# Performance work log

Measured on AMD Instinct MI355X. Metric: run time of the kernel, lower is better.

## Reference

```python
import jax, jax.numpy as jnp
import numpy as np

D = 1024
H = 16
DH = D // H  # 64


def setup_inputs() -> dict:
    key = jax.random.key(0)
    ks = jax.random.split(key, 7)
    X = jax.random.normal(ks[0], (2, 2048, D), dtype=jnp.float32)
    # Per-head projection weights stacked along head axis: [H, D, DH]
    s = 1.0 / np.sqrt(D)
    Wq = jax.random.uniform(ks[1], (H, D, DH), jnp.float32, -s, s)
    Wk = jax.random.uniform(ks[2], (H, D, DH), jnp.float32, -s, s)
    Wv = jax.random.uniform(ks[3], (H, D, DH), jnp.float32, -s, s)
    bq = jax.random.uniform(ks[4], (H, DH), jnp.float32, -s, s)
    bk = jax.random.uniform(ks[5], (H, DH), jnp.float32, -s, s)
    bv = jax.random.uniform(ks[6], (H, DH), jnp.float32, -s, s)
    return {"X": X, "Wq": Wq, "bq": bq, "Wk": Wk, "bk": bk, "Wv": Wv, "bv": bv}


def reference(X, Wq, bq, Wk, bk, Wv, bv):
    B, S, _ = X.shape
    # Per-head linear projections (batched over heads): [B, H, S, DH]
    Q = jnp.einsum('bsd,hde->bhse', X, Wq) + bq[None, :, None, :]
    K = jnp.einsum('bsd,hde->bhse', X, Wk) + bk[None, :, None, :]
    V = jnp.einsum('bsd,hde->bhse', X, Wv) + bv[None, :, None, :]
    scale = jnp.sqrt(jnp.asarray(DH, dtype=X.dtype))
    QK = jnp.einsum('bhse,bhte->bhst', Q, K) / scale  # [B, H, S, S]
    # Faithful to source: softmax over full row FIRST, then lower-tri mask
    # (post-softmax tril, no renormalization).
    sQK = jax.nn.softmax(QK, axis=-1)
    tril = jnp.tril(jnp.ones((S, S), dtype=X.dtype))
    sQK = sQK * tril
    out = jnp.einsum('bhst,bhte->bhse', sQK, V)  # [B, H, S, DH]
    # Concatenate heads along feature dim (torch.cat over per-head outputs)
    return out.transpose(0, 2, 1, 3).reshape(B, S, H * DH)
```

## Files before the change

### kernel.cpp

```cpp
#include <hip/hip_runtime.h>
#include <math.h>

#define B_  2
#define S_  2048
#define D_  1024
#define H_  16
#define DH_ 64

typedef unsigned short u16;
typedef unsigned int   u32;
typedef _Float16       f16;
typedef _Float16 half8  __attribute__((ext_vector_type(8)));
typedef _Float16 half4  __attribute__((ext_vector_type(4)));
typedef float    f32x4  __attribute__((ext_vector_type(4)));

#if __has_builtin(__builtin_amdgcn_exp2f)
#define EXP2(x) __builtin_amdgcn_exp2f(x)
#else
#define EXP2(x) exp2f(x)
#endif

__device__ __forceinline__ u16 h_bits(f16 h){ return __builtin_bit_cast(u16, h); }

__global__ __launch_bounds__(256) void prep_kernel(
    const float* __restrict__ X,
    const float* __restrict__ Wq, const float* __restrict__ Wk,
    const float* __restrict__ Wv,
    u16* __restrict__ Xhi, u16* __restrict__ Xlo, u16* __restrict__ Wt)
{
    __shared__ float Wf[64][65];
    const int bid = blockIdx.x;
    const int c   = threadIdx.x;

    if (bid < 4096){
        const int idx = bid * 256 + c;
        float4 v = ((const float4*)X)[idx];
        float fv[4] = {v.x, v.y, v.z, v.w};
        u16 hh[4], ll[4];
        #pragma unroll
        for (int j = 0; j < 4; ++j){
            f16 hi = (f16)fv[j];
            hh[j] = h_bits(hi);
            ll[j] = h_bits((f16)(fv[j] - (float)hi));
        }
        uint2 ph, pl;
        ph.x = hh[0] | ((u32)hh[1] << 16);
        ph.y = hh[2] | ((u32)hh[3] << 16);
        pl.x = ll[0] | ((u32)ll[1] << 16);
        pl.y = ll[2] | ((u32)ll[3] << 16);
        ((uint2*)Xhi)[idx] = ph;
        ((uint2*)Xlo)[idx] = pl;
        return;
    }

    const int wb = bid - 4096;
    const int d0 = (wb & 15) * 64;
    const int h  = (wb >> 4) & 15;
    const int which = wb >> 8;
    const float* src = (which == 0) ? Wq : (which == 1) ? Wk : Wv;
    src += (size_t)h * D_ * DH_;

    #pragma unroll
    for (int it = 0; it < 4; ++it){
        int d  = (c >> 4) + 16 * it;
        int e4 = (c & 15) * 4;
        float4 v = *(const float4*)(src + (size_t)(d0 + d) * DH_ + e4);
        Wf[d][e4+0] = v.x; Wf[d][e4+1] = v.y; Wf[d][e4+2] = v.z; Wf[d][e4+3] = v.w;
    }
    __syncthreads();
    u16* dst = Wt + (size_t)(which * H_ + h) * DH_ * D_;
    #pragma unroll
    for (int it = 0; it < 4; ++it){
        int e  = (c >> 4) + 16 * it;
        int d4 = (c & 15) * 4;
        u16 q[4];
        #pragma unroll
        for (int j = 0; j < 4; ++j)
            q[j] = h_bits((f16)(Wf[d4 + j][e] * 64.0f));
        u32* p = (u32*)(dst + (size_t)e * D_ + d0 + d4);
        p[0] = q[0] | ((u32)q[1] << 16);
        p[1] = q[2] | ((u32)q[3] << 16);
    }
}

#define PKS 40

__global__ __launch_bounds__(256, 3) void proj_kernel(
    const u16* __restrict__ Xhi, const u16* __restrict__ Xlo,
    const u16* __restrict__ Wt,
    const float* __restrict__ bq, const float* __restrict__ bk,
    const float* __restrict__ bv,
    f16* __restrict__ Qh, f16* __restrict__ Kh, f16* __restrict__ Vt)
{
    __shared__ u16 XsHi[128 * PKS], XsLo[128 * PKS], Bs[128 * PKS];

    const int tid  = threadIdx.x;
    const int lane = tid & 63;
    const int w    = tid >> 6;
    const int quad = lane >> 4;
    const int ln   = lane & 15;
    const int wr   = (w >> 1) * 64;
    const int wc   = (w & 1) * 64;
    const int m0   = blockIdx.x * 128;
    const int c0   = blockIdx.y * 128;

    const int sr  = tid >> 2;
    const int sch = (tid & 3) * 8;

    const u16* xh0 = Xhi + (size_t)(m0 + sr) * D_ + sch;
    const u16* xh1 = xh0 + (size_t)64 * D_;
    const u16* xl0 = Xlo + (size_t)(m0 + sr) * D_ + sch;
    const u16* xl1 = xl0 + (size_t)64 * D_;
    const u16* wb0 = Wt  + (size_t)(c0 + sr) * D_ + sch;
    const u16* wb1 = wb0 + (size_t)64 * D_;

    uint4 rh0 = *(const uint4*)xh0, rh1 = *(const uint4*)xh1;
    uint4 rl0 = *(const uint4*)xl0, rl1 = *(const uint4*)xl1;
    uint4 rw0 = *(const uint4*)wb0, rw1 = *(const uint4*)wb1;

    f32x4 acc[4][4];
    #pragma unroll
    for (int i = 0; i < 4; ++i)
        #pragma unroll
        for (int j = 0; j < 4; ++j)
            acc[i][j] = (f32x4){0.f, 0.f, 0.f, 0.f};

    for (int k0 = 0; k0 < D_; k0 += 32){
        __syncthreads();
        *(uint4*)&XsHi[sr * PKS + sch]        = rh0;
        *(uint4*)&XsHi[(sr + 64) * PKS + sch] = rh1;
        *(uint4*)&XsLo[sr * PKS + sch]        = rl0;
        *(uint4*)&XsLo[(sr + 64) * PKS + sch] = rl1;
        *(uint4*)&Bs[sr * PKS + sch]          = rw0;
        *(uint4*)&Bs[(sr + 64) * PKS + sch]   = rw1;
        const int kn = k0 + 32;
        if (kn < D_){
            rh0 = *(const uint4*)(xh0 + kn); rh1 = *(const uint4*)(xh1 + kn);
            rl0 = *(const uint4*)(xl0 + kn); rl1 = *(const uint4*)(xl1 + kn);
            rw0 = *(const uint4*)(wb0 + kn); rw1 = *(const uint4*)(wb1 + kn);
        }
        __syncthreads();

        half8 ahi[4], alo[4], bf[4];
        #pragma unroll
        for (int mt = 0; mt < 4; ++mt){
            int row = wr + 16 * mt + ln;
            ahi[mt] = __builtin_bit_cast(half8, *(const uint4*)&XsHi[row * PKS + quad * 8]);
            alo[mt] = __builtin_bit_cast(half8, *(const uint4*)&XsLo[row * PKS + quad * 8]);
        }
        #pragma unroll
        for (int nt = 0; nt < 4; ++nt)
            bf[nt] = __builtin_bit_cast(half8,
                *(const uint4*)&Bs[(wc + 16 * nt + ln) * PKS + quad * 8]);
        #pragma unroll
        for (int mt = 0; mt < 4; ++mt)
            #pragma unroll
            for (int nt = 0; nt < 4; ++nt){
                acc[mt][nt] = __builtin_amdgcn_mfma_f32_16x16x32_f16(ahi[mt], bf[nt], acc[mt][nt], 0, 0, 0);
                acc[mt][nt] = __builtin_amdgcn_mfma_f32_16x16x32_f16(alo[mt], bf[nt], acc[mt][nt], 0, 0, 0);
            }
    }

    const float QSCALE = 0.125f * 1.44269504088896340736f;
    const float INV64  = 0.015625f;
    #pragma unroll
    for (int nt = 0; nt < 4; ++nt){
        int colg  = c0 + wc + 16 * nt + ln;
        int which = colg >> 10;
        int h     = (colg >> 6) & 15;
        int e     = colg & 63;
        const float* bp = (which == 0) ? bq : (which == 1) ? bk : bv;
        float bias = bp[h * DH_ + e];
        if (which < 2){
            f16* op = (which == 0) ? Qh : Kh;
            float scale = (which == 0) ? QSCALE : 1.0f;
            #pragma unroll
            for (int mt = 0; mt < 4; ++mt)
                #pragma unroll
                for (int r = 0; r < 4; ++r){
                    int sg = m0 + wr + 16 * mt + 4 * quad + r;
                    int b  = sg >> 11;
                    int s  = sg & (S_ - 1);
                    float val = (acc[mt][nt][r] * INV64 + bias) * scale;
                    op[((size_t)(b * H_ + h) * S_ + s) * DH_ + e] = (f16)val;
                }
        } else {
            #pragma unroll
            for (int mt = 0; mt < 4; ++mt){
                int sg0 = m0 + wr + 16 * mt + 4 * quad;
                int b   = sg0 >> 11;
                int s0  = sg0 & (S_ - 1);
                u16 p[4];
                #pragma unroll
                for (int r = 0; r < 4; ++r)
                    p[r] = h_bits((f16)(acc[mt][nt][r] * INV64 + bias));
                uint2 pk;
                pk.x = p[0] | ((u32)p[1] << 16);
                pk.y = p[2] | ((u32)p[3] << 16);
                *(uint2*)((u16*)Vt + ((size_t)((b * H_ + h) * DH_ + e)) * S_ + s0) = pk;
            }
        }
    }
}

#define AKS 72

__global__ __launch_bounds__(256, 4) void attn_kernel(
    const f16* __restrict__ Qh, const f16* __restrict__ Kh,
    const f16* __restrict__ Vt, float* __restrict__ Out)
{
    __shared__ u16 Ks[64 * AKS];
    __shared__ u16 Vs[64 * AKS];

    const int tid  = threadIdx.x;
    const int lane = tid & 63;
    const int w    = tid >> 6;
    const int quad = lane >> 4;
    const int ln   = lane & 15;
    const int hb   = blockIdx.x;
    const int i    = blockIdx.y;
    const int h    = hb & 15;
    const int b    = hb >> 4;
    const int bh   = hb;
    const int sub  = w & 1;
    const int qbase = (w >> 1) ? (S_ - 32 * (i + 1) + 16 * sub)
                               : (32 * i + 16 * sub);
    const int vmax  = S_ - 32 * i - 1;

    const u16* Qg = (const u16*)Qh + (size_t)bh * S_ * DH_;
    const u16* Kg = (const u16*)Kh + (size_t)bh * S_ * DH_;
    const u16* Vg = (const u16*)Vt + (size_t)bh * DH_ * S_;

    half8 qf[2];
    #pragma unroll
    for (int ks = 0; ks < 2; ++ks)
        qf[ks] = __builtin_bit_cast(half8,
            *(const uint4*)(Qg + (size_t)(qbase + ln) * DH_ + 32 * ks + 8 * quad));

    const int kr = tid >> 3;
    const int kc = (tid & 7) * 8;

    uint4 kA = *(const uint4*)(Kg + (size_t)kr * DH_ + kc);
    uint4 kB = *(const uint4*)(Kg + (size_t)(kr + 32) * DH_ + kc);
    uint4 vA = *(const uint4*)(Vg + (size_t)kr * S_ + kc);
    uint4 vB = *(const uint4*)(Vg + (size_t)(kr + 32) * S_ + kc);

    float l_r = 0.f;
    f32x4 o_acc[4];
    #pragma unroll
    for (int nt = 0; nt < 4; ++nt) o_acc[nt] = (f32x4){0.f, 0.f, 0.f, 0.f};

    const int qrow   = qbase + ln;
    const int pv_lim = qbase + 15;

    for (int t0 = 0; t0 < S_; t0 += 64){
        __syncthreads();
        *(uint4*)&Ks[kr * AKS + kc]        = kA;
        *(uint4*)&Ks[(kr + 32) * AKS + kc] = kB;
        if (t0 <= vmax){
            *(uint4*)&Vs[kr * AKS + kc]        = vA;
            *(uint4*)&Vs[(kr + 32) * AKS + kc] = vB;
        }
        const int tn = t0 + 64;
        if (tn < S_){
            kA = *(const uint4*)(Kg + (size_t)(tn + kr) * DH_ + kc);
            kB = *(const uint4*)(Kg + (size_t)(tn + kr + 32) * DH_ + kc);
            if (tn <= vmax){
                vA = *(const uint4*)(Vg + (size_t)kr * S_ + tn + kc);
                vB = *(const uint4*)(Vg + (size_t)(kr + 32) * S_ + tn + kc);
            }
        }
        __syncthreads();

        f32x4 sc[4];
        #pragma unroll
        for (int mt = 0; mt < 4; ++mt) sc[mt] = (f32x4){0.f, 0.f, 0.f, 0.f};
        #pragma unroll
        for (int ks = 0; ks < 2; ++ks)
            #pragma unroll
            for (int mt = 0; mt < 4; ++mt){
                half8 kf = __builtin_bit_cast(half8,
                    *(const uint4*)&Ks[(16 * mt + ln) * AKS + 32 * ks + 8 * quad]);
                sc[mt] = __builtin_amdgcn_mfma_f32_16x16x32_f16(kf, qf[ks], sc[mt], 0, 0, 0);
            }

        #pragma unroll
        for (int mt = 0; mt < 4; ++mt)
            #pragma unroll
            for (int r = 0; r < 4; ++r)
                sc[mt][r] = EXP2(sc[mt][r]);
        float s = ((sc[0][0] + sc[0][1] + sc[0][2] + sc[0][3]) +
                   (sc[1][0] + sc[1][1] + sc[1][2] + sc[1][3])) +
                  ((sc[2][0] + sc[2][1] + sc[2][2] + sc[2][3]) +
                   (sc[3][0] + sc[3][1] + sc[3][2] + sc[3][3]));
        s += __shfl_xor(s, 16);
        s += __shfl_xor(s, 32);
        l_r += s;

        #pragma unroll
        for (int mt = 0; mt < 4; ++mt){
            const int ts = t0 + 16 * mt;
            if (ts <= pv_lim){
                half4 pf;
                if (ts == qbase){
                    int tb = ts + 4 * quad;
                    #pragma unroll
                    for (int r = 0; r < 4; ++r)
                        pf[r] = (tb + r > qrow) ? (f16)0.f : (f16)sc[mt][r];
                } else {
                    #pragma unroll
                    for (int r = 0; r < 4; ++r)
                        pf[r] = (f16)sc[mt][r];
                }
                #pragma unroll
                for (int nt = 0; nt < 4; ++nt){
                    half4 vf = __builtin_bit_cast(half4,
                        *(const uint2*)&Vs[(16 * nt + ln) * AKS + 16 * mt + 4 * quad]);
                    o_acc[nt] = __builtin_amdgcn_mfma_f32_16x16x16f16(pf, vf, o_acc[nt], 0, 0, 0);
                }
            }
        }
    }

    #pragma unroll
    for (int r = 0; r < 4; ++r){
        float lv  = __shfl(l_r, (lane & 48) | (4 * quad + r));
        float inv = 1.0f / lv;
        int sg = qbase + 4 * quad + r;
        float* op = Out + ((size_t)b * S_ + sg) * D_ + h * DH_;
        #pragma unroll
        for (int nt = 0; nt < 4; ++nt)
            op[16 * nt + ln] = o_acc[nt][r] * inv;
    }
}

extern "C" void kernel_launch(void* const* d_in, const int* in_sizes, int n_in,
                              void* d_out, int out_size, void* d_ws, size_t ws_size,
                              hipStream_t stream)
{
    const float* X  = (const float*)d_in[0];
    const float* Wq = (const float*)d_in[1];
    const float* bq = (const float*)d_in[2];
    const float* Wk = (const float*)d_in[3];
    const float* bk = (const float*)d_in[4];
    const float* Wv = (const float*)d_in[5];
    const float* bv = (const float*)d_in[6];
    float* out = (float*)d_out;

    u16* Wt  = (u16*)d_ws;
    f16* Qh  = (f16*)(Wt + 3145728);
    f16* Kh  = Qh + 4194304;
    f16* Vt  = Kh + 4194304;
    u16* Xhi = (u16*)(Vt + 4194304);
    u16* Xlo = Xhi + 4194304;

    prep_kernel<<<dim3(4096 + 768), 256, 0, stream>>>(X, Wq, Wk, Wv, Xhi, Xlo, Wt);
    proj_kernel<<<dim3(32, 24), 256, 0, stream>>>(Xhi, Xlo, Wt, bq, bk, bv, Qh, Kh, Vt);
    attn_kernel<<<dim3(32, 32), 256, 0, stream>>>(Qh, Kh, Vt, out);
}
```

Baseline: 189.2 us.

## Restructure projection GEMM with 256x256 tiles and direct-to-LDS double-buffered loads

The projection kernel now uses 512-thread blocks that each compute a 256x256 output tile, and a 1D grid with a block-index swizzle. Tiles are staged straight into XOR-swizzled LDS with global_load_lds, double-buffered across K steps, with explicit vmcnt waits, raw barriers and raised wave priority around MFMA bursts. The hi and lo halves of X are handled as one concatenated K loop. The goal is more data reuse per loaded byte and fewer LDS bank conflicts. In exchange, 128KB of LDS per block and only 192 blocks may leave many CUs idle.

```diff
diff --git a/kernel.cpp b/kernel.cpp
--- a/kernel.cpp
+++ b/kernel.cpp
@@ -83,89 +83,153 @@
     }
 }
 
-#define PKS 40
-
-__global__ __launch_bounds__(256, 3) void proj_kernel(
+__device__ __forceinline__ void gload16(const void* g, void* l){
+    __builtin_amdgcn_global_load_lds(
+        (const __attribute__((address_space(1))) void*)g,
+        (__attribute__((address_space(3))) void*)l, 16, 0, 0);
+}
+
+__device__ __forceinline__ half8 frag16(const char* hb, int row, int quad){
+    int off = row * 64 + ((quad * 16) ^ ((row & 6) << 3));
+    return __builtin_bit_cast(half8, *(const uint4*)(hb + off));
+}
+
+#define FENCE() asm volatile("" ::: "memory")
+#define BARX()  do{ FENCE(); __builtin_amdgcn_s_barrier(); FENCE(); }while(0)
+#define WAIT_VM4() asm volatile("s_waitcnt vmcnt(4)" ::: "memory")
+#define WAIT_VM0() asm volatile("s_waitcnt vmcnt(0)" ::: "memory")
+
+#define STAGE_A(t_, kh_) do{ \
+    const int _t = (t_); \
+    const int _gk = ((_t & 15) << 6) + ((kh_) << 5); \
+    const u16* _g0 = ((_t < 16) ? xa0h : xa0l) + _gk; \
+    const u16* _g1 = ((_t < 16) ? xa1h : xa1l) + _gk; \
+    char* _l = AsB + ((_t & 1) << 15) + ((kh_) << 14); \
+    gload16(_g0, _l + ldw0); \
+    gload16(_g1, _l + ldw1); \
+}while(0)
+
+#define STAGE_B(t_, kh_) do{ \
+    const int _t = (t_); \
+    const int _gk = ((_t & 15) << 6) + ((kh_) << 5); \
+    char* _l = BsB + ((_t & 1) << 15) + ((kh_) << 14); \
+    gload16(wb0 + _gk, _l + ldw0); \
+    gload16(wb1 + _gk, _l + ldw1); \
+}while(0)
+
+#define READ_B(bh_) do{ \
+    _Pragma("unroll") \
+    for (int nf_ = 0; nf_ < 4; ++nf_) \
+        bfr[nf_] = frag16((bh_), wn * 64 + nf_ * 16 + ln, quad); \
+}while(0)
+
+#define READ_A(ah_, mbase_) do{ \
+    _Pragma("unroll") \
+    for (int mi_ = 0; mi_ < 4; ++mi_) \
+        af[mi_] = frag16((ah_), wm * 128 + ((mbase_) + mi_) * 16 + ln, quad); \
+}while(0)
+
+#define MFMA_BLOCK(mbase_) do{ \
+    BARX(); \
+    asm volatile("s_waitcnt lgkmcnt(0)" ::: "memory"); \
+    __builtin_amdgcn_sched_barrier(0); \
+    __builtin_amdgcn_s_setprio(1); \
+    _Pragma("unroll") \
+    for (int mi_ = 0; mi_ < 4; ++mi_){ \
+        _Pragma("unroll") \
+        for (int nf_ = 0; nf_ < 4; ++nf_) \
+            acc[(mbase_) + mi_][nf_] = __builtin_amdgcn_mfma_f32_16x16x32_f16( \
+                af[mi_], bfr[nf_], acc[(mbase_) + mi_][nf_], 0, 0, 0); \
+    } \
+    __builtin_amdgcn_s_setprio(0); \
+}while(0)
+
+__global__ __launch_bounds__(512, 2) void proj_kernel(
     const u16* __restrict__ Xhi, const u16* __restrict__ Xlo,
     const u16* __restrict__ Wt,
     const float* __restrict__ bq, const float* __restrict__ bk,
     const float* __restrict__ bv,
     f16* __restrict__ Qh, f16* __restrict__ Kh, f16* __restrict__ Vt)
 {
-    __shared__ u16 XsHi[128 * PKS], XsLo[128 * PKS], Bs[128 * PKS];
+    __shared__ __align__(16) char AsB[65536];
+    __shared__ __align__(16) char BsB[65536];
 
     const int tid  = threadIdx.x;
     const int lane = tid & 63;
     const int w    = tid >> 6;
+    const int wm   = w >> 2;
+    const int wn   = w & 3;
     const int quad = lane >> 4;
     const int ln   = lane & 15;
-    const int wr   = (w >> 1) * 64;
-    const int wc   = (w & 1) * 64;
-    const int m0   = blockIdx.x * 128;
-    const int c0   = blockIdx.y * 128;
-
-    const int sr  = tid >> 2;
-    const int sch = (tid & 3) * 8;
-
-    const u16* xh0 = Xhi + (size_t)(m0 + sr) * D_ + sch;
-    const u16* xh1 = xh0 + (size_t)64 * D_;
-    const u16* xl0 = Xlo + (size_t)(m0 + sr) * D_ + sch;
-    const u16* xl1 = xl0 + (size_t)64 * D_;
-    const u16* wb0 = Wt  + (size_t)(c0 + sr) * D_ + sch;
-    const u16* wb1 = wb0 + (size_t)64 * D_;
-
-    uint4 rh0 = *(const uint4*)xh0, rh1 = *(const uint4*)xh1;
-    uint4 rl0 = *(const uint4*)xl0, rl1 = *(const uint4*)xl1;
-    uint4 rw0 = *(const uint4*)wb0, rw1 = *(const uint4*)wb1;
-
-    f32x4 acc[4][4];
-    #pragma unroll
-    for (int i = 0; i < 4; ++i)
+
+    const int bid = blockIdx.x;
+    const int swz = (bid & 7) * 24 + (bid >> 3);
+    const int m0  = (swz / 12) * 256;
+    const int c0  = (swz % 12) * 256;
+
+    const int Lr0 = w * 1024 + lane * 16;
+    const int Lr1 = (8 + w) * 1024 + lane * 16;
+    const int P0  = Lr0 ^ (((Lr0 >> 7) & 3) << 4);
+    const int P1  = Lr1 ^ (((Lr1 >> 7) & 3) << 4);
+    const int row0 = P0 >> 6,        row1 = P1 >> 6;
+    const int ko0  = (P0 & 63) >> 1, ko1  = (P1 & 63) >> 1;
+
+    const u16* xa0h = Xhi + (size_t)(m0 + row0) * D_ + ko0;
+    const u16* xa1h = Xhi + (size_t)(m0 + row1) * D_ + ko1;
+    const u16* xa0l = Xlo + (size_t)(m0 + row0) * D_ + ko0;
+    const u16* xa1l = Xlo + (size_t)(m0 + row1) * D_ + ko1;
+    const u16* wb0  = Wt  + (size_t)(c0 + row0) * D_ + ko0;
+    const u16* wb1  = Wt  + (size_t)(c0 + row1) * D_ + ko1;
+
+    const int ldw0 = w * 1024;
+    const int ldw1 = (8 + w) * 1024;
+
+    f32x4 acc[8][4];
+    #pragma unroll
+    for (int i = 0; i < 8; ++i)
         #pragma unroll
         for (int j = 0; j < 4; ++j)
             acc[i][j] = (f32x4){0.f, 0.f, 0.f, 0.f};
 
-    for (int k0 = 0; k0 < D_; k0 += 32){
-        __syncthreads();
-        *(uint4*)&XsHi[sr * PKS + sch]        = rh0;
-        *(uint4*)&XsHi[(sr + 64) * PKS + sch] = rh1;
-        *(uint4*)&XsLo[sr * PKS + sch]        = rl0;
-        *(uint4*)&XsLo[(sr + 64) * PKS + sch] = rl1;
-        *(uint4*)&Bs[sr * PKS + sch]          = rw0;
-        *(uint4*)&Bs[(sr + 64) * PKS + sch]   = rw1;
-        const int kn = k0 + 32;
-        if (kn < D_){
-            rh0 = *(const uint4*)(xh0 + kn); rh1 = *(const uint4*)(xh1 + kn);
-            rl0 = *(const uint4*)(xl0 + kn); rl1 = *(const uint4*)(xl1 + kn);
-            rw0 = *(const uint4*)(wb0 + kn); rw1 = *(const uint4*)(wb1 + kn);
-        }
-        __syncthreads();
-
-        half8 ahi[4], alo[4], bf[4];
-        #pragma unroll
-        for (int mt = 0; mt < 4; ++mt){
-            int row = wr + 16 * mt + ln;
-            ahi[mt] = __builtin_bit_cast(half8, *(const uint4*)&XsHi[row * PKS + quad * 8]);
-            alo[mt] = __builtin_bit_cast(half8, *(const uint4*)&XsLo[row * PKS + quad * 8]);
-        }
-        #pragma unroll
-        for (int nt = 0; nt < 4; ++nt)
-            bf[nt] = __builtin_bit_cast(half8,
-                *(const uint4*)&Bs[(wc + 16 * nt + ln) * PKS + quad * 8]);
-        #pragma unroll
-        for (int mt = 0; mt < 4; ++mt)
-            #pragma unroll
-            for (int nt = 0; nt < 4; ++nt){
-                acc[mt][nt] = __builtin_amdgcn_mfma_f32_16x16x32_f16(ahi[mt], bf[nt], acc[mt][nt], 0, 0, 0);
-                acc[mt][nt] = __builtin_amdgcn_mfma_f32_16x16x32_f16(alo[mt], bf[nt], acc[mt][nt], 0, 0, 0);
-            }
+    STAGE_A(0, 0); STAGE_B(0, 0); STAGE_A(0, 1); STAGE_B(0, 1);
+    STAGE_A(1, 0); STAGE_B(1, 0);
+    WAIT_VM4();
+    BARX();
+
+    half8 bfr[4], af[4];
+
+    #pragma unroll 2
+    for (int t = 0; t < 32; ++t){
+        const char* Ah = AsB + ((t & 1) << 15);
+        const char* Bh = BsB + ((t & 1) << 15);
+
+        READ_B(Bh); READ_A(Ah, 0);
+        if (t < 31) STAGE_A(t + 1, 1);
+        MFMA_BLOCK(0);
+        BARX();
+
+        READ_A(Ah, 4);
+        if (t < 31) STAGE_B(t + 1, 1);
+        MFMA_BLOCK(4);
+        BARX();
+
+        READ_B(Bh + 16384); READ_A(Ah + 16384, 0);
+        if (t < 30) STAGE_A(t + 2, 0);
+        MFMA_BLOCK(0);
+        BARX();
+
+        READ_A(Ah + 16384, 4);
+        if (t < 30) STAGE_B(t + 2, 0);
+        MFMA_BLOCK(4);
+        if (t < 30) { WAIT_VM4(); } else { WAIT_VM0(); }
+        BARX();
     }
 
     const float QSCALE = 0.125f * 1.44269504088896340736f;
     const float INV64  = 0.015625f;
     #pragma unroll
-    for (int nt = 0; nt < 4; ++nt){
-        int colg  = c0 + wc + 16 * nt + ln;
+    for (int nf = 0; nf < 4; ++nf){
+        int colg  = c0 + wn * 64 + nf * 16 + ln;
         int which = colg >> 10;
         int h     = (colg >> 6) & 15;
         int e     = colg & 63;
@@ -175,25 +239,25 @@
             f16* op = (which == 0) ? Qh : Kh;
             float scale = (which == 0) ? QSCALE : 1.0f;
             #pragma unroll
-            for (int mt = 0; mt < 4; ++mt)
+            for (int mf = 0; mf < 8; ++mf)
                 #pragma unroll
                 for (int r = 0; r < 4; ++r){
-                    int sg = m0 + wr + 16 * mt + 4 * quad + r;
+                    int sg = m0 + wm * 128 + mf * 16 + 4 * quad + r;
                     int b  = sg >> 11;
                     int s  = sg & (S_ - 1);
-                    float val = (acc[mt][nt][r] * INV64 + bias) * scale;
+                    float val = (acc[mf][nf][r] * INV64 + bias) * scale;
                     op[((size_t)(b * H_ + h) * S_ + s) * DH_ + e] = (f16)val;
                 }
         } else {
             #pragma unroll
-            for (int mt = 0; mt < 4; ++mt){
-                int sg0 = m0 + wr + 16 * mt + 4 * quad;
+            for (int mf = 0; mf < 8; ++mf){
+                int sg0 = m0 + wm * 128 + mf * 16 + 4 * quad;
                 int b   = sg0 >> 11;
                 int s0  = sg0 & (S_ - 1);
                 u16 p[4];
                 #pragma unroll
                 for (int r = 0; r < 4; ++r)
-                    p[r] = h_bits((f16)(acc[mt][nt][r] * INV64 + bias));
+                    p[r] = h_bits((f16)(acc[mf][nf][r] * INV64 + bias));
                 uint2 pk;
                 pk.x = p[0] | ((u32)p[1] << 16);
                 pk.y = p[2] | ((u32)p[3] << 16);
@@ -355,6 +419,6 @@
     u16* Xlo = Xhi + 4194304;
 
     prep_kernel<<<dim3(4096 + 768), 256, 0, stream>>>(X, Wq, Wk, Wv, Xhi, Xlo, Wt);
-    proj_kernel<<<dim3(32, 24), 256, 0, stream>>>(Xhi, Xlo, Wt, bq, bk, bv, Qh, Kh, Vt);
+    proj_kernel<<<dim3(192), dim3(512), 0, stream>>>(Xhi, Xlo, Wt, bq, bk, bv, Qh, Kh, Vt);
     attn_kernel<<<dim3(32, 32), 256, 0, stream>>>(Qh, Kh, Vt, out);
 }
```

New measurement: 199.4 us. 1.05x slower.

## Process 32 query rows per wave in attention to reuse K/V tiles

Applied to the files above, without the earlier changes.

Each wave in the attention kernel now handles two 16-row query groups instead of one. Each K fragment read from shared memory feeds two QK MFMAs, and each V fragment feeds two PV MFMAs. The grid is halved and launch bounds drop to 2 blocks per CU to make room for the doubled accumulators. This lowers the number of K/V global loads and LDS reads per unit of work, at the cost of fewer resident waves and fewer blocks (512) to spread across CUs.

```diff
diff --git a/kernel.cpp b/kernel.cpp
--- a/kernel.cpp
+++ b/kernel.cpp
@@ -205,7 +205,7 @@
 
 #define AKS 72
 
-__global__ __launch_bounds__(256, 4) void attn_kernel(
+__global__ __launch_bounds__(256, 2) void attn_kernel(
     const f16* __restrict__ Qh, const f16* __restrict__ Kh,
     const f16* __restrict__ Vt, float* __restrict__ Out)
 {
@@ -223,19 +223,22 @@
     const int b    = hb >> 4;
     const int bh   = hb;
     const int sub  = w & 1;
-    const int qbase = (w >> 1) ? (S_ - 32 * (i + 1) + 16 * sub)
-                               : (32 * i + 16 * sub);
-    const int vmax  = S_ - 32 * i - 1;
+    const int qbase = (w >> 1) ? (S_ - 64 * (i + 1) + 32 * sub)
+                               : (64 * i + 32 * sub);
+    const int vmax  = S_ - 64 * i - 1;
 
     const u16* Qg = (const u16*)Qh + (size_t)bh * S_ * DH_;
     const u16* Kg = (const u16*)Kh + (size_t)bh * S_ * DH_;
     const u16* Vg = (const u16*)Vt + (size_t)bh * DH_ * S_;
 
-    half8 qf[2];
-    #pragma unroll
-    for (int ks = 0; ks < 2; ++ks)
-        qf[ks] = __builtin_bit_cast(half8,
+    half8 qf0[2], qf1[2];
+    #pragma unroll
+    for (int ks = 0; ks < 2; ++ks){
+        qf0[ks] = __builtin_bit_cast(half8,
             *(const uint4*)(Qg + (size_t)(qbase + ln) * DH_ + 32 * ks + 8 * quad));
+        qf1[ks] = __builtin_bit_cast(half8,
+            *(const uint4*)(Qg + (size_t)(qbase + 16 + ln) * DH_ + 32 * ks + 8 * quad));
+    }
 
     const int kr = tid >> 3;
     const int kc = (tid & 7) * 8;
@@ -245,13 +248,18 @@
     uint4 vA = *(const uint4*)(Vg + (size_t)kr * S_ + kc);
     uint4 vB = *(const uint4*)(Vg + (size_t)(kr + 32) * S_ + kc);
 
-    float l_r = 0.f;
-    f32x4 o_acc[4];
-    #pragma unroll
-    for (int nt = 0; nt < 4; ++nt) o_acc[nt] = (f32x4){0.f, 0.f, 0.f, 0.f};
-
-    const int qrow   = qbase + ln;
-    const int pv_lim = qbase + 15;
+    float l0 = 0.f, l1 = 0.f;
+    f32x4 oa0[4], oa1[4];
+    #pragma unroll
+    for (int nt = 0; nt < 4; ++nt){
+        oa0[nt] = (f32x4){0.f, 0.f, 0.f, 0.f};
+        oa1[nt] = (f32x4){0.f, 0.f, 0.f, 0.f};
+    }
+
+    const int qrow0 = qbase + ln;
+    const int qrow1 = qbase + 16 + ln;
+    const int pvl0  = qbase + 15;
+    const int pvl1  = qbase + 31;
 
     for (int t0 = 0; t0 < S_; t0 += 64){
         __syncthreads();
@@ -272,51 +280,82 @@
         }
         __syncthreads();
 
-        f32x4 sc[4];
-        #pragma unroll
-        for (int mt = 0; mt < 4; ++mt) sc[mt] = (f32x4){0.f, 0.f, 0.f, 0.f};
+        f32x4 s0[4], s1[4];
+        #pragma unroll
+        for (int mt = 0; mt < 4; ++mt){
+            s0[mt] = (f32x4){0.f, 0.f, 0.f, 0.f};
+            s1[mt] = (f32x4){0.f, 0.f, 0.f, 0.f};
+        }
         #pragma unroll
         for (int ks = 0; ks < 2; ++ks)
             #pragma unroll
             for (int mt = 0; mt < 4; ++mt){
                 half8 kf = __builtin_bit_cast(half8,
                     *(const uint4*)&Ks[(16 * mt + ln) * AKS + 32 * ks + 8 * quad]);
-                sc[mt] = __builtin_amdgcn_mfma_f32_16x16x32_f16(kf, qf[ks], sc[mt], 0, 0, 0);
+                s0[mt] = __builtin_amdgcn_mfma_f32_16x16x32_f16(kf, qf0[ks], s0[mt], 0, 0, 0);
+                s1[mt] = __builtin_amdgcn_mfma_f32_16x16x32_f16(kf, qf1[ks], s1[mt], 0, 0, 0);
             }
 
         #pragma unroll
         for (int mt = 0; mt < 4; ++mt)
             #pragma unroll
-            for (int r = 0; r < 4; ++r)
-                sc[mt][r] = EXP2(sc[mt][r]);
-        float s = ((sc[0][0] + sc[0][1] + sc[0][2] + sc[0][3]) +
-                   (sc[1][0] + sc[1][1] + sc[1][2] + sc[1][3])) +
-                  ((sc[2][0] + sc[2][1] + sc[2][2] + sc[2][3]) +
-                   (sc[3][0] + sc[3][1] + sc[3][2] + sc[3][3]));
-        s += __shfl_xor(s, 16);
-        s += __shfl_xor(s, 32);
-        l_r += s;
+            for (int r = 0; r < 4; ++r){
+                s0[mt][r] = EXP2(s0[mt][r]);
+                s1[mt][r] = EXP2(s1[mt][r]);
+            }
+        {
+            float sa = ((s0[0][0] + s0[0][1] + s0[0][2] + s0[0][3]) +
+                        (s0[1][0] + s0[1][1] + s0[1][2] + s0[1][3])) +
+                       ((s0[2][0] + s0[2][1] + s0[2][2] + s0[2][3]) +
+                        (s0[3][0] + s0[3][1] + s0[3][2] + s0[3][3]));
+            sa += __shfl_xor(sa, 16);
+            sa += __shfl_xor(sa, 32);
+            l0 += sa;
+            float sb = ((s1[0][0] + s1[0][1] + s1[0][2] + s1[0][3]) +
+                        (s1[1][0] + s1[1][1] + s1[1][2] + s1[1][3])) +
+                       ((s1[2][0] + s1[2][1] + s1[2][2] + s1[2][3]) +
+                        (s1[3][0] + s1[3][1] + s1[3][2] + s1[3][3]));
+            sb += __shfl_xor(sb, 16);
+            sb += __shfl_xor(sb, 32);
+            l1 += sb;
+        }
 
         #pragma unroll
         for (int mt = 0; mt < 4; ++mt){
             const int ts = t0 + 16 * mt;
-            if (ts <= pv_lim){
-                half4 pf;
-                if (ts == qbase){
+            if (ts <= pvl1){
+                const int g0on = (ts <= pvl0);
+                half4 pf1;
+                if (ts == qbase + 16){
                     int tb = ts + 4 * quad;
                     #pragma unroll
                     for (int r = 0; r < 4; ++r)
-                        pf[r] = (tb + r > qrow) ? (f16)0.f : (f16)sc[mt][r];
+                        pf1[r] = (tb + r > qrow1) ? (f16)0.f : (f16)s1[mt][r];
                 } else {
                     #pragma unroll
                     for (int r = 0; r < 4; ++r)
-                        pf[r] = (f16)sc[mt][r];
+                        pf1[r] = (f16)s1[mt][r];
+                }
+                half4 pf0;
+                if (g0on){
+                    if (ts == qbase){
+                        int tb = ts + 4 * quad;
+                        #pragma unroll
+                        for (int r = 0; r < 4; ++r)
+                            pf0[r] = (tb + r > qrow0) ? (f16)0.f : (f16)s0[mt][r];
+                    } else {
+                        #pragma unroll
+                        for (int r = 0; r < 4; ++r)
+                            pf0[r] = (f16)s0[mt][r];
+                    }
                 }
                 #pragma unroll
                 for (int nt = 0; nt < 4; ++nt){
                     half4 vf = __builtin_bit_cast(half4,
                         *(const uint2*)&Vs[(16 * nt + ln) * AKS + 16 * mt + 4 * quad]);
-                    o_acc[nt] = __builtin_amdgcn_mfma_f32_16x16x16f16(pf, vf, o_acc[nt], 0, 0, 0);
+                    oa1[nt] = __builtin_amdgcn_mfma_f32_16x16x16f16(pf1, vf, oa1[nt], 0, 0, 0);
+                    if (g0on)
+                        oa0[nt] = __builtin_amdgcn_mfma_f32_16x16x16f16(pf0, vf, oa0[nt], 0, 0, 0);
                 }
             }
         }
@@ -324,13 +363,21 @@
 
     #pragma unroll
     for (int r = 0; r < 4; ++r){
-        float lv  = __shfl(l_r, (lane & 48) | (4 * quad + r));
-        float inv = 1.0f / lv;
-        int sg = qbase + 4 * quad + r;
-        float* op = Out + ((size_t)b * S_ + sg) * D_ + h * DH_;
+        float lv0  = __shfl(l0, (lane & 48) | (4 * quad + r));
+        float inv0 = 1.0f / lv0;
+        int sg0 = qbase + 4 * quad + r;
+        float* op0 = Out + ((size_t)b * S_ + sg0) * D_ + h * DH_;
         #pragma unroll
         for (int nt = 0; nt < 4; ++nt)
-            op[16 * nt + ln] = o_acc[nt][r] * inv;
+            op0[16 * nt + ln] = oa0[nt][r] * inv0;
+
+        float lv1  = __shfl(l1, (lane & 48) | (4 * quad + r));
+        float inv1 = 1.0f / lv1;
+        int sg1 = qbase + 16 + 4 * quad + r;
+        float* op1 = Out + ((size_t)b * S_ + sg1) * D_ + h * DH_;
+        #pragma unroll
+        for (int nt = 0; nt < 4; ++nt)
+            op1[16 * nt + ln] = oa1[nt][r] * inv1;
     }
 }
 
@@ -356,5 +403,5 @@
 
     prep_kernel<<<dim3(4096 + 768), 256, 0, stream>>>(X, Wq, Wk, Wv, Xhi, Xlo, Wt);
     proj_kernel<<<dim3(32, 24), 256, 0, stream>>>(Xhi, Xlo, Wt, bq, bk, bv, Qh, Kh, Vt);
-    attn_kernel<<<dim3(32, 32), 256, 0, stream>>>(Qh, Kh, Vt, out);
+    attn_kernel<<<dim3(32, 16), 256, 0, stream>>>(Qh, Kh, Vt, out);
 }
```

Measured after the change: 230.3 us. 21.7% more time.

## Double-buffer K/V shared tiles with one barrier per iteration and MFMA priority

Applied to the files above, without the earlier changes.

Splits the K and V shared-memory tiles into two buffers so each iteration writes the next tile into the idle buffer while computing on the current one. This drops one of the two barriers per iteration and pushes the register prefetch one more tile ahead. It also raises wave priority around the QK MFMA block with s_setprio. The cost is twice the LDS per block, which may lower occupancy at four blocks per CU, and more live registers from prefetching further ahead.

```diff
diff --git a/kernel.cpp b/kernel.cpp
--- a/kernel.cpp
+++ b/kernel.cpp
@@ -209,8 +209,8 @@
     const f16* __restrict__ Qh, const f16* __restrict__ Kh,
     const f16* __restrict__ Vt, float* __restrict__ Out)
 {
-    __shared__ u16 Ks[64 * AKS];
-    __shared__ u16 Vs[64 * AKS];
+    __shared__ u16 Ks[2][64 * AKS];
+    __shared__ u16 Vs[2][64 * AKS];
 
     const int tid  = threadIdx.x;
     const int lane = tid & 63;
@@ -245,6 +245,21 @@
     uint4 vA = *(const uint4*)(Vg + (size_t)kr * S_ + kc);
     uint4 vB = *(const uint4*)(Vg + (size_t)(kr + 32) * S_ + kc);
 
+    *(uint4*)&Ks[0][kr * AKS + kc]        = kA;
+    *(uint4*)&Ks[0][(kr + 32) * AKS + kc] = kB;
+    *(uint4*)&Vs[0][kr * AKS + kc]        = vA;
+    *(uint4*)&Vs[0][(kr + 32) * AKS + kc] = vB;
+
+    {
+        const int tn = 64;
+        kA = *(const uint4*)(Kg + (size_t)(tn + kr) * DH_ + kc);
+        kB = *(const uint4*)(Kg + (size_t)(tn + kr + 32) * DH_ + kc);
+        if (tn <= vmax){
+            vA = *(const uint4*)(Vg + (size_t)kr * S_ + tn + kc);
+            vB = *(const uint4*)(Vg + (size_t)(kr + 32) * S_ + tn + kc);
+        }
+    }
+
     float l_r = 0.f;
     f32x4 o_acc[4];
     #pragma unroll
@@ -254,35 +269,46 @@
     const int pv_lim = qbase + 15;
 
     for (int t0 = 0; t0 < S_; t0 += 64){
+        const int cur = (t0 >> 6) & 1;
+        const u16* Kc = Ks[cur];
+        const u16* Vc = Vs[cur];
+        u16* Kn = Ks[cur ^ 1];
+        u16* Vn = Vs[cur ^ 1];
+
         __syncthreads();
-        *(uint4*)&Ks[kr * AKS + kc]        = kA;
-        *(uint4*)&Ks[(kr + 32) * AKS + kc] = kB;
-        if (t0 <= vmax){
-            *(uint4*)&Vs[kr * AKS + kc]        = vA;
-            *(uint4*)&Vs[(kr + 32) * AKS + kc] = vB;
-        }
+
         const int tn = t0 + 64;
         if (tn < S_){
-            kA = *(const uint4*)(Kg + (size_t)(tn + kr) * DH_ + kc);
-            kB = *(const uint4*)(Kg + (size_t)(tn + kr + 32) * DH_ + kc);
+            *(uint4*)&Kn[kr * AKS + kc]        = kA;
+            *(uint4*)&Kn[(kr + 32) * AKS + kc] = kB;
             if (tn <= vmax){
-                vA = *(const uint4*)(Vg + (size_t)kr * S_ + tn + kc);
-                vB = *(const uint4*)(Vg + (size_t)(kr + 32) * S_ + tn + kc);
-            }
-        }
-        __syncthreads();
+                *(uint4*)&Vn[kr * AKS + kc]        = vA;
+                *(uint4*)&Vn[(kr + 32) * AKS + kc] = vB;
+            }
+        }
+        const int tp = t0 + 128;
+        if (tp < S_){
+            kA = *(const uint4*)(Kg + (size_t)(tp + kr) * DH_ + kc);
+            kB = *(const uint4*)(Kg + (size_t)(tp + kr + 32) * DH_ + kc);
+            if (tp <= vmax){
+                vA = *(const uint4*)(Vg + (size_t)kr * S_ + tp + kc);
+                vB = *(const uint4*)(Vg + (size_t)(kr + 32) * S_ + tp + kc);
+            }
+        }
 
         f32x4 sc[4];
         #pragma unroll
         for (int mt = 0; mt < 4; ++mt) sc[mt] = (f32x4){0.f, 0.f, 0.f, 0.f};
+        __builtin_amdgcn_s_setprio(1);
         #pragma unroll
         for (int ks = 0; ks < 2; ++ks)
             #pragma unroll
             for (int mt = 0; mt < 4; ++mt){
                 half8 kf = __builtin_bit_cast(half8,
-                    *(const uint4*)&Ks[(16 * mt + ln) * AKS + 32 * ks + 8 * quad]);
+                    *(const uint4*)&Kc[(16 * mt + ln) * AKS + 32 * ks + 8 * quad]);
                 sc[mt] = __builtin_amdgcn_mfma_f32_16x16x32_f16(kf, qf[ks], sc[mt], 0, 0, 0);
             }
+        __builtin_amdgcn_s_setprio(0);
 
         #pragma unroll
         for (int mt = 0; mt < 4; ++mt)
@@ -315,7 +341,7 @@
                 #pragma unroll
                 for (int nt = 0; nt < 4; ++nt){
                     half4 vf = __builtin_bit_cast(half4,
-                        *(const uint2*)&Vs[(16 * nt + ln) * AKS + 16 * mt + 4 * quad]);
+                        *(const uint2*)&Vc[(16 * nt + ln) * AKS + 16 * mt + 4 * quad]);
                     o_acc[nt] = __builtin_amdgcn_mfma_f32_16x16x16f16(pf, vf, o_acc[nt], 0, 0, 0);
                 }
             }
```

New measurement: 195.2 us. 1.03x slower.
